# Kernel tuning notes

Hardware: AMD Instinct MI355X
Metric: run time of the kernel (lower is better)

The kernel has to match this reference:

```python
import jax, jax.numpy as jnp
import numpy as np

B, S, E, NH = 1, 2048, 1024, 8
DH = E // NH
EPS = 1e-6


def setup_inputs() -> dict:
    key = jax.random.key(0)
    ks = jax.random.split(key, 7)
    q = jax.random.normal(ks[0], (B, S, E), dtype=jnp.float32)
    k = jax.random.normal(ks[1], (B, S, E), dtype=jnp.float32)
    v = jax.random.normal(ks[2], (B, S, E), dtype=jnp.float32)
    # gate projections (original inits kernel=0; use small random to keep math non-degenerate)
    Wi = jax.random.normal(ks[3], (3 * E, NH), dtype=jnp.float32) * 0.02
    bi = jax.random.normal(ks[4], (NH,), dtype=jnp.float32) * 0.1
    Wf = jax.random.normal(ks[5], (3 * E, NH), dtype=jnp.float32) * 0.02
    bf = jnp.linspace(3.0, 6.0, NH, dtype=jnp.float32)  # bias_linspace_initializer(3,6)
    ln_scale = jnp.ones((E,), dtype=jnp.float32)
    return {"q": q, "k": k, "v": v, "Wi": Wi, "bi": bi, "Wf": Wf, "bf": bf, "ln_scale": ln_scale}


def _mlstm_forward(q, k, v, Wi, bi, Wf, bf, ln_scale):
    # gate preactivations: (B, NH, S, 1)
    gate_in = jnp.concatenate([q, k, v], axis=-1)  # (B, S, 3E)
    i_pre = jnp.transpose(gate_in @ Wi + bi, (0, 2, 1))[..., None]
    f_pre = jnp.transpose(gate_in @ Wf + bf, (0, 2, 1))[..., None]

    # heads: (B, NH, S, DH)
    qh = jnp.transpose(q.reshape(B, S, NH, DH), (0, 2, 1, 3))
    kh = jnp.transpose(k.reshape(B, S, NH, DH), (0, 2, 1, 3))
    vh = jnp.transpose(v.reshape(B, S, NH, DH), (0, 2, 1, 3))

    # cumulative log forget gates -> decay matrix fm[i,j] = sum_{t=j+1..i} log_sigmoid(f_t)
    log_fg = jax.nn.log_sigmoid(f_pre)                  # (B, NH, S, 1)
    cum = jnp.cumsum(log_fg, axis=2)[..., 0]            # (B, NH, S)
    fm = cum[:, :, :, None] - cum[:, :, None, :]        # (B, NH, S, S)

    mask = jnp.tril(jnp.ones((S, S), dtype=bool))
    log_D = jnp.where(mask, fm + i_pre[..., 0][:, :, None, :], -jnp.inf)  # + igate of column j

    max_log_D = jnp.max(log_D, axis=-1, keepdims=True)  # row-wise stabilizer (B, NH, S, 1)
    D = jnp.exp(log_D - max_log_D)

    qk = jnp.einsum("bhsd,bhtd->bhst", qh, kh) / jnp.sqrt(jnp.float32(DH))
    C = qk * D
    normalizer = jnp.maximum(jnp.abs(C.sum(axis=-1, keepdims=True)), jnp.exp(-max_log_D))
    h = jnp.einsum("bhst,bhtd->bhsd", C / (normalizer + EPS), vh)  # (B, NH, S, DH)

    # per-head layernorm over DH, scale of size E reshaped per head, no bias
    mu = h.mean(axis=-1, keepdims=True)
    var = h.var(axis=-1, keepdims=True)
    h_norm = (h - mu) * jax.lax.rsqrt(var + EPS) * ln_scale.reshape(1, NH, 1, DH)

    return jnp.transpose(h_norm, (0, 2, 1, 3)).reshape(B, S, E)


def reference(q, k, v, Wi, bi, Wf, bf, ln_scale):
    return _mlstm_forward(q, k, v, Wi, bi, Wf, bf, ln_scale)
```

## Files before the change

kernel.cpp:

```cpp
#include <hip/hip_runtime.h>
#include <math.h>

namespace {
constexpr int S  = 2048;
constexpr int E  = 1024;
constexpr int NH = 8;
constexpr int DH = 128;
constexpr float EPSF = 1e-6f;
constexpr float INV_LN2 = 1.4426950408889634f;
}

typedef short short8 __attribute__((ext_vector_type(8)));
typedef float f32x16 __attribute__((ext_vector_type(16)));
typedef float f32x4  __attribute__((ext_vector_type(4)));

__device__ __forceinline__ unsigned short f2bf(float x) {
  unsigned int u = __float_as_uint(x);
  unsigned int r = (u + 0x7fffu + ((u >> 16) & 1u)) >> 16;
  return (unsigned short)r;
}

__device__ __forceinline__ void async_copy16(const void* g, void* l) {
  __builtin_amdgcn_global_load_lds(
      (const __attribute__((address_space(1))) unsigned int*)g,
      (__attribute__((address_space(3))) unsigned int*)l, 16, 0, 0);
}

__global__ __launch_bounds__(256) void convert_kernel(
    const float* __restrict__ q, const float* __restrict__ k, const float* __restrict__ v,
    const float* __restrict__ Wi, const float* __restrict__ Wf,
    unsigned short* __restrict__ qb, unsigned short* __restrict__ kb,
    unsigned short* __restrict__ vt, unsigned short* __restrict__ wt2)
{
  const int b = blockIdx.x;
  const int tid = threadIdx.x;
  if (b < 512) {
    __shared__ float Ts[64][65];
    const int j0 = (b & 31) * 64;
    const int d0 = ((b >> 5) & 1) * 64;
    const int h  = b >> 6;
    const int c = tid & 63, r4 = tid >> 6;
    #pragma unroll
    for (int rr = 0; rr < 16; ++rr) {
      int r = r4*16 + rr;
      Ts[r][c] = v[(size_t)(j0 + r)*E + h*DH + d0 + c];
    }
    __syncthreads();
    #pragma unroll
    for (int rr = 0; rr < 16; ++rr) {
      int r = r4*16 + rr;
      vt[(size_t)(h*DH + d0 + r)*S + j0 + c] = f2bf(Ts[c][r]);
    }
  } else if (b < 1024) {
    const int bb = b - 512;
    constexpr int N4 = S*E/4;
    const float4* src = (bb < 256) ? (const float4*)q : (const float4*)k;
    ushort4* dst = (bb < 256) ? (ushort4*)qb : (ushort4*)kb;
    const int b0 = (bb & 255);
    for (int i = b0*256 + tid; i < N4; i += 256*256) {
      float4 x = src[i];
      ushort4 o;
      o.x = f2bf(x.x); o.y = f2bf(x.y); o.z = f2bf(x.z); o.w = f2bf(x.w);
      dst[i] = o;
    }
  } else {
    for (int idx = tid; idx < 16*3*E; idx += 256) {
      int n = idx / (3*E), e = idx - n*(3*E);
      float val = (n < 8) ? Wi[e*NH + n] : Wf[e*NH + (n-8)];
      wt2[idx] = f2bf(val);
    }
  }
}

__global__ __launch_bounds__(256) void gates_kernel(
    const float* __restrict__ q, const float* __restrict__ k, const float* __restrict__ v,
    const unsigned short* __restrict__ wt2, float* __restrict__ partial)
{
  const int mt = blockIdx.x, p = blockIdx.y;
  const float* src = (p == 0) ? q : (p == 1) ? k : v;
  const int wv = threadIdx.x >> 6, lane = threadIdx.x & 63;
  const int m0 = (mt*4 + wv)*16;
  const int tr = lane & 15;
  const int ks = (lane >> 4) * 8;
  f32x4 acc = {0.f, 0.f, 0.f, 0.f};
  for (int e0 = 0; e0 < E; e0 += 32) {
    const float* ap = src + (size_t)(m0 + tr)*E + e0 + ks;
    float4 a0 = *reinterpret_cast<const float4*>(ap);
    float4 a1 = *reinterpret_cast<const float4*>(ap + 4);
    short8 af;
    af[0] = (short)f2bf(a0.x); af[1] = (short)f2bf(a0.y);
    af[2] = (short)f2bf(a0.z); af[3] = (short)f2bf(a0.w);
    af[4] = (short)f2bf(a1.x); af[5] = (short)f2bf(a1.y);
    af[6] = (short)f2bf(a1.z); af[7] = (short)f2bf(a1.w);
    short8 bf8 = *reinterpret_cast<const short8*>(wt2 + (size_t)tr*(3*E) + p*E + e0 + ks);
    acc = __builtin_amdgcn_mfma_f32_16x16x32_bf16(af, bf8, acc, 0, 0, 0);
  }
  const int n = lane & 15, rbase = (lane >> 4) * 4;
  #pragma unroll
  for (int r = 0; r < 4; ++r)
    partial[(size_t)(p*16 + n)*S + m0 + rbase + r] = acc[r];
}

__global__ __launch_bounds__(256) void scan_kernel(
    const float* __restrict__ partial,
    const float* __restrict__ bi, const float* __restrict__ bfg,
    float* __restrict__ a2_out, float* __restrict__ m2_out)
{
  const int h = blockIdx.x, tid = threadIdx.x;
  const int lane = tid & 63, wv = tid >> 6;
  constexpr int PER = S / 256;
  const int bt = tid * PER;
  __shared__ float wred[4], wmax[4];

  float ipv[PER], c[PER];
  float run = 0.f;
  #pragma unroll
  for (int u = 0; u < PER; u++) {
    int t = bt + u;
    float ip = bi[h], fp = bfg[h];
    #pragma unroll
    for (int p = 0; p < 3; ++p) {
      ip += partial[(size_t)(p*16 + h)*S + t];
      fp += partial[(size_t)(p*16 + 8 + h)*S + t];
    }
    ipv[u] = ip;
    float ls = fminf(fp, 0.f) - log1pf(__expf(-fabsf(fp)));
    run += ls; c[u] = run;
  }
  float s = run;
  #pragma unroll
  for (int off = 1; off < 64; off <<= 1) {
    float t = __shfl_up(s, off);
    if (lane >= off) s += t;
  }
  if (lane == 63) wred[wv] = s;
  __syncthreads();
  float wpre = 0.f;
  for (int i = 0; i < wv; i++) wpre += wred[i];
  const float excl = wpre + (s - run);

  float av[PER], mloc[PER];
  float lm = -INFINITY;
  #pragma unroll
  for (int u = 0; u < PER; u++) {
    c[u] += excl;
    av[u] = ipv[u] - c[u];
    lm = fmaxf(lm, av[u]);
    mloc[u] = lm;
  }
  float sm_ = lm;
  #pragma unroll
  for (int off = 1; off < 64; off <<= 1) {
    float t = __shfl_up(sm_, off);
    if (lane >= off) sm_ = fmaxf(sm_, t);
  }
  if (lane == 63) wmax[wv] = sm_;
  __syncthreads();
  float wpm = -INFINITY;
  for (int i = 0; i < wv; i++) wpm = fmaxf(wpm, wmax[i]);
  float prev = __shfl_up(sm_, 1);
  if (lane == 0) prev = -INFINITY;
  const float exclm = fmaxf(wpm, prev);
  #pragma unroll
  for (int u = 0; u < PER; u++) {
    float m = fmaxf(exclm, mloc[u]);
    a2_out[h*S + bt + u] = av[u] * INV_LN2;
    m2_out[h*S + bt + u] = m * INV_LN2;
  }
}

__global__ __launch_bounds__(256, 2) void attn_kernel(
    const unsigned short* __restrict__ qb, const unsigned short* __restrict__ kb,
    const unsigned short* __restrict__ vt,
    const float* __restrict__ a2g, const float* __restrict__ m2g,
    const float* __restrict__ ln, float* __restrict__ out)
{
  const int qt = 63 - (int)(blockIdx.x >> 3);
  const int h  = blockIdx.x & 7;
  const int tid = threadIdx.x;
  const int w = tid >> 6, lane = tid & 63, l31 = lane & 31, half = lane >> 5;
  const int qi0 = qt * 32;
  const int niter = (qt + 4) >> 2;
  const int jcol_off = 32*w + l31;

  __shared__ short Klds[128*128];
  __shared__ short Vlds[128*128];
  __shared__ short Psm[32*136];
  __shared__ float mrow[32];
  float* Hs = (float*)Klds;

  if (tid < 32) mrow[tid] = m2g[h*S + qi0 + tid];

  short8 qf[8];
  #pragma unroll
  for (int s = 0; s < 8; ++s)
    qf[s] = *reinterpret_cast<const short8*>(
        qb + (size_t)(qi0 + l31)*E + h*DH + 16*s + 8*half);

  __syncthreads();
  float mreg[16];
  #pragma unroll
  for (int r = 0; r < 16; ++r) mreg[r] = mrow[(r&3) + 8*(r>>2) + 4*half];

  f32x16 acc = {0,0,0,0,0,0,0,0,0,0,0,0,0,0,0,0};

  const int lrow4 = lane >> 4;
  const int jb    = lane & 15;
  const int kq_row = 32*w + l31;
  const int kq_swz = kq_row & 15;

  for (int jt = 0; jt < niter; ++jt) {
    const int j0 = jt * 128;
    __syncthreads();

    #pragma unroll
    for (int i = 0; i < 8; ++i) {
      const int ii  = w*8 + i;
      const int row = ii*4 + lrow4;
      const int cc  = jb ^ (row & 15);
      async_copy16(kb + (size_t)(j0 + row)*E + h*DH + cc*8, &Klds[ii*512]);
      async_copy16(vt + (size_t)(h*DH + row)*S + j0 + cc*8, &Vlds[ii*512]);
    }
    const float ajv = a2g[h*S + j0 + jcol_off];
    __syncthreads();

    f32x16 qk = {0,0,0,0,0,0,0,0,0,0,0,0,0,0,0,0};
    #pragma unroll
    for (int s = 0; s < 8; ++s) {
      short8 kf = *reinterpret_cast<const short8*>(
          &Klds[kq_row*128 + ((2*s + half) ^ kq_swz) * 8]);
      qk = __builtin_amdgcn_mfma_f32_32x32x16_bf16(qf[s], kf, qk, 0, 0, 0);
    }
    const int jcol = j0 + jcol_off;
    #pragma unroll
    for (int r = 0; r < 16; ++r) {
      const int iloc = (r&3) + 8*(r>>2) + 4*half;
      float pv = (jcol <= qi0 + iloc) ? qk[r] * exp2f(ajv - mreg[r]) : 0.f;
      Psm[iloc*136 + jcol_off] = (short)f2bf(pv);
    }
    __syncthreads();

    #pragma unroll
    for (int s = 0; s < 8; ++s) {
      short8 pf = *reinterpret_cast<const short8*>(&Psm[l31*136 + 16*s + 8*half]);
      short8 vf = *reinterpret_cast<const short8*>(
          &Vlds[kq_row*128 + ((2*s + half) ^ kq_swz) * 8]);
      acc = __builtin_amdgcn_mfma_f32_32x32x16_bf16(pf, vf, acc, 0, 0, 0);
    }
  }

  __syncthreads();
  #pragma unroll
  for (int r = 0; r < 16; ++r)
    Hs[((r&3) + 8*(r>>2) + 4*half)*132 + 32*w + l31] = acc[r];
  __syncthreads();
  {
    const int row = tid >> 3, seg = tid & 7;
    float vals[16];
    #pragma unroll
    for (int c4 = 0; c4 < 4; ++c4) {
      float4 v4 = *reinterpret_cast<const float4*>(&Hs[row*132 + seg*16 + c4*4]);
      vals[c4*4+0]=v4.x; vals[c4*4+1]=v4.y; vals[c4*4+2]=v4.z; vals[c4*4+3]=v4.w;
    }
    float s1 = 0.f, s2 = 0.f;
    #pragma unroll
    for (int c = 0; c < 16; ++c) { s1 += vals[c]; s2 = fmaf(vals[c], vals[c], s2); }
    #pragma unroll
    for (int off = 1; off < 8; off <<= 1) {
      s1 += __shfl_xor(s1, off);
      s2 += __shfl_xor(s2, off);
    }
    const float mu = s1 * (1.f/128.f);
    float var = fmaxf(s2 * (1.f/128.f) - mu*mu, 0.f);
    const float rs = rsqrtf(var + EPSF);
    const size_t ob = (size_t)(qi0 + row)*E + h*DH + seg*16;
    #pragma unroll
    for (int c = 0; c < 16; ++c)
      out[ob + c] = (vals[c] - mu) * rs * ln[h*DH + seg*16 + c];
  }
}

extern "C" void kernel_launch(void* const* d_in, const int* in_sizes, int n_in,
                              void* d_out, int out_size, void* d_ws, size_t ws_size,
                              hipStream_t stream) {
  const float* q  = (const float*)d_in[0];
  const float* k  = (const float*)d_in[1];
  const float* v  = (const float*)d_in[2];
  const float* Wi = (const float*)d_in[3];
  const float* bi = (const float*)d_in[4];
  const float* Wf = (const float*)d_in[5];
  const float* bf = (const float*)d_in[6];
  const float* ln = (const float*)d_in[7];
  float* out = (float*)d_out;

  char* base = (char*)d_ws;
  unsigned short* qb  = (unsigned short*)(base);
  unsigned short* kb  = (unsigned short*)(base + (size_t)S*E*2);
  unsigned short* vt  = (unsigned short*)(base + (size_t)S*E*4);
  unsigned short* wt2 = (unsigned short*)(base + (size_t)S*E*6);
  float* partial = (float*)(base + (size_t)S*E*6 + 16*3*E*2);
  float* a2 = partial + (size_t)48*S;
  float* m2 = a2 + NH*S;

  convert_kernel<<<dim3(1025), dim3(256), 0, stream>>>(q, k, v, Wi, Wf, qb, kb, vt, wt2);
  gates_kernel<<<dim3(32, 3), dim3(256), 0, stream>>>(q, k, v, wt2, partial);
  scan_kernel<<<dim3(NH), dim3(256), 0, stream>>>(partial, bi, bf, a2, m2);
  attn_kernel<<<dim3(512), dim3(256), 0, stream>>>(qb, kb, vt, a2, m2, ln, out);
}
```

Baseline: 159.6 us.

## Split long causal attention rows across two blocks and combine partials

Query tiles in the upper half (qt>=32) are now split into two blocks that each process half of the key tiles. Each half writes an unnormalized partial output, and a new combine kernel sums the two halves and applies the layernorm. This evens out per-block work along the causal triangle. The gates kernel now loops over q, k and v itself and writes ipre and log-sigmoid values directly, which shortens the scan. The weight transpose is spread across 16 blocks. The costs are an extra launch and a round trip of the partial outputs through global memory.

```diff
diff --git a/kernel.cpp b/kernel.cpp
--- a/kernel.cpp
+++ b/kernel.cpp
@@ -64,69 +64,70 @@
       dst[i] = o;
     }
   } else {
-    for (int idx = tid; idx < 16*3*E; idx += 256) {
-      int n = idx / (3*E), e = idx - n*(3*E);
+    const int n = b - 1024;
+    for (int e = tid; e < 3*E; e += 256) {
       float val = (n < 8) ? Wi[e*NH + n] : Wf[e*NH + (n-8)];
-      wt2[idx] = f2bf(val);
+      wt2[(size_t)n*(3*E) + e] = f2bf(val);
     }
   }
 }
 
 __global__ __launch_bounds__(256) void gates_kernel(
     const float* __restrict__ q, const float* __restrict__ k, const float* __restrict__ v,
-    const unsigned short* __restrict__ wt2, float* __restrict__ partial)
-{
-  const int mt = blockIdx.x, p = blockIdx.y;
-  const float* src = (p == 0) ? q : (p == 1) ? k : v;
+    const unsigned short* __restrict__ wt2,
+    const float* __restrict__ bi, const float* __restrict__ bfg,
+    float* __restrict__ ipre, float* __restrict__ lsf)
+{
   const int wv = threadIdx.x >> 6, lane = threadIdx.x & 63;
-  const int m0 = (mt*4 + wv)*16;
+  const int m0 = (blockIdx.x*4 + wv)*16;
   const int tr = lane & 15;
   const int ks = (lane >> 4) * 8;
   f32x4 acc = {0.f, 0.f, 0.f, 0.f};
-  for (int e0 = 0; e0 < E; e0 += 32) {
-    const float* ap = src + (size_t)(m0 + tr)*E + e0 + ks;
-    float4 a0 = *reinterpret_cast<const float4*>(ap);
-    float4 a1 = *reinterpret_cast<const float4*>(ap + 4);
-    short8 af;
-    af[0] = (short)f2bf(a0.x); af[1] = (short)f2bf(a0.y);
-    af[2] = (short)f2bf(a0.z); af[3] = (short)f2bf(a0.w);
-    af[4] = (short)f2bf(a1.x); af[5] = (short)f2bf(a1.y);
-    af[6] = (short)f2bf(a1.z); af[7] = (short)f2bf(a1.w);
-    short8 bf8 = *reinterpret_cast<const short8*>(wt2 + (size_t)tr*(3*E) + p*E + e0 + ks);
-    acc = __builtin_amdgcn_mfma_f32_16x16x32_bf16(af, bf8, acc, 0, 0, 0);
+  const float* srcs[3] = {q, k, v};
+  #pragma unroll
+  for (int p = 0; p < 3; ++p) {
+    const float* src = srcs[p];
+    for (int e0 = 0; e0 < E; e0 += 32) {
+      const float* ap = src + (size_t)(m0 + tr)*E + e0 + ks;
+      float4 a0 = *reinterpret_cast<const float4*>(ap);
+      float4 a1 = *reinterpret_cast<const float4*>(ap + 4);
+      short8 af;
+      af[0] = (short)f2bf(a0.x); af[1] = (short)f2bf(a0.y);
+      af[2] = (short)f2bf(a0.z); af[3] = (short)f2bf(a0.w);
+      af[4] = (short)f2bf(a1.x); af[5] = (short)f2bf(a1.y);
+      af[6] = (short)f2bf(a1.z); af[7] = (short)f2bf(a1.w);
+      short8 bf8 = *reinterpret_cast<const short8*>(wt2 + (size_t)tr*(3*E) + p*E + e0 + ks);
+      acc = __builtin_amdgcn_mfma_f32_16x16x32_bf16(af, bf8, acc, 0, 0, 0);
+    }
   }
   const int n = lane & 15, rbase = (lane >> 4) * 4;
   #pragma unroll
-  for (int r = 0; r < 4; ++r)
-    partial[(size_t)(p*16 + n)*S + m0 + rbase + r] = acc[r];
+  for (int r = 0; r < 4; ++r) {
+    int t = m0 + rbase + r;
+    float val = acc[r];
+    if (n < 8) {
+      ipre[n*S + t] = val + bi[n];
+    } else {
+      float fp = val + bfg[n-8];
+      lsf[(n-8)*S + t] = fminf(fp, 0.f) - log1pf(__expf(-fabsf(fp)));
+    }
+  }
 }
 
 __global__ __launch_bounds__(256) void scan_kernel(
-    const float* __restrict__ partial,
-    const float* __restrict__ bi, const float* __restrict__ bfg,
+    const float* __restrict__ ipre, const float* __restrict__ lsf,
     float* __restrict__ a2_out, float* __restrict__ m2_out)
 {
   const int h = blockIdx.x, tid = threadIdx.x;
   const int lane = tid & 63, wv = tid >> 6;
   constexpr int PER = S / 256;
-  const int bt = tid * PER;
+  const int base = h*S + tid*PER;
   __shared__ float wred[4], wmax[4];
 
-  float ipv[PER], c[PER];
+  float c[PER];
   float run = 0.f;
   #pragma unroll
-  for (int u = 0; u < PER; u++) {
-    int t = bt + u;
-    float ip = bi[h], fp = bfg[h];
-    #pragma unroll
-    for (int p = 0; p < 3; ++p) {
-      ip += partial[(size_t)(p*16 + h)*S + t];
-      fp += partial[(size_t)(p*16 + 8 + h)*S + t];
-    }
-    ipv[u] = ip;
-    float ls = fminf(fp, 0.f) - log1pf(__expf(-fabsf(fp)));
-    run += ls; c[u] = run;
-  }
+  for (int u = 0; u < PER; u++) { run += lsf[base+u]; c[u] = run; }
   float s = run;
   #pragma unroll
   for (int off = 1; off < 64; off <<= 1) {
@@ -144,7 +145,7 @@
   #pragma unroll
   for (int u = 0; u < PER; u++) {
     c[u] += excl;
-    av[u] = ipv[u] - c[u];
+    av[u] = ipre[base+u] - c[u];
     lm = fmaxf(lm, av[u]);
     mloc[u] = lm;
   }
@@ -164,8 +165,8 @@
   #pragma unroll
   for (int u = 0; u < PER; u++) {
     float m = fmaxf(exclm, mloc[u]);
-    a2_out[h*S + bt + u] = av[u] * INV_LN2;
-    m2_out[h*S + bt + u] = m * INV_LN2;
+    a2_out[base+u] = av[u] * INV_LN2;
+    m2_out[base+u] = m * INV_LN2;
   }
 }
 
@@ -173,14 +174,20 @@
     const unsigned short* __restrict__ qb, const unsigned short* __restrict__ kb,
     const unsigned short* __restrict__ vt,
     const float* __restrict__ a2g, const float* __restrict__ m2g,
-    const float* __restrict__ ln, float* __restrict__ out)
-{
-  const int qt = 63 - (int)(blockIdx.x >> 3);
-  const int h  = blockIdx.x & 7;
+    const float* __restrict__ ln, float* __restrict__ opart, float* __restrict__ out)
+{
+  const int b = blockIdx.x;
+  int h, qt, part;
+  if (b < 512) { h = b & 7; qt = 63 - (b >> 3); part = 0; }
+  else { int i = b - 512; h = i & 7; qt = 63 - (i >> 3); part = 1; }
+  const int nspl = (qt >= 32) ? 2 : 1;
+  const int N = (qt + 4) >> 2;
+  const int jt_lo = (part == 1) ? (N >> 1) : 0;
+  const int jt_hi = (nspl == 2 && part == 0) ? (N >> 1) : N;
+
   const int tid = threadIdx.x;
   const int w = tid >> 6, lane = tid & 63, l31 = lane & 31, half = lane >> 5;
   const int qi0 = qt * 32;
-  const int niter = (qt + 4) >> 2;
   const int jcol_off = 32*w + l31;
 
   __shared__ short Klds[128*128];
@@ -209,10 +216,9 @@
   const int kq_row = 32*w + l31;
   const int kq_swz = kq_row & 15;
 
-  for (int jt = 0; jt < niter; ++jt) {
+  for (int jt = jt_lo; jt < jt_hi; ++jt) {
     const int j0 = jt * 128;
     __syncthreads();
-
     #pragma unroll
     for (int i = 0; i < 8; ++i) {
       const int ii  = w*8 + i;
@@ -239,7 +245,6 @@
       Psm[iloc*136 + jcol_off] = (short)f2bf(pv);
     }
     __syncthreads();
-
     #pragma unroll
     for (int s = 0; s < 8; ++s) {
       short8 pf = *reinterpret_cast<const short8*>(&Psm[l31*136 + 16*s + 8*half]);
@@ -249,6 +254,16 @@
     }
   }
 
+  if (nspl == 2) {
+    float* dst = opart + ((size_t)((qt - 32)*8 + h)*2 + part)*(32*128);
+    #pragma unroll
+    for (int r = 0; r < 16; ++r) {
+      const int iloc = (r&3) + 8*(r>>2) + 4*half;
+      dst[iloc*128 + 32*w + l31] = acc[r];
+    }
+    return;
+  }
+
   __syncthreads();
   #pragma unroll
   for (int r = 0; r < 16; ++r)
@@ -278,6 +293,42 @@
     for (int c = 0; c < 16; ++c)
       out[ob + c] = (vals[c] - mu) * rs * ln[h*DH + seg*16 + c];
   }
+}
+
+__global__ __launch_bounds__(256) void combine_kernel(
+    const float* __restrict__ opart, const float* __restrict__ ln,
+    float* __restrict__ out)
+{
+  const int t = blockIdx.x;
+  const int qt = 32 + (t >> 3);
+  const int h  = t & 7;
+  const float* p0 = opart + (size_t)((qt - 32)*8 + h)*2*(32*128);
+  const float* p1 = p0 + 32*128;
+  const int tid = threadIdx.x;
+  const int row = tid >> 3, seg = tid & 7;
+  float vals[16];
+  #pragma unroll
+  for (int c4 = 0; c4 < 4; ++c4) {
+    float4 a = *reinterpret_cast<const float4*>(&p0[row*128 + seg*16 + c4*4]);
+    float4 b = *reinterpret_cast<const float4*>(&p1[row*128 + seg*16 + c4*4]);
+    vals[c4*4+0] = a.x + b.x; vals[c4*4+1] = a.y + b.y;
+    vals[c4*4+2] = a.z + b.z; vals[c4*4+3] = a.w + b.w;
+  }
+  float s1 = 0.f, s2 = 0.f;
+  #pragma unroll
+  for (int c = 0; c < 16; ++c) { s1 += vals[c]; s2 = fmaf(vals[c], vals[c], s2); }
+  #pragma unroll
+  for (int off = 1; off < 8; off <<= 1) {
+    s1 += __shfl_xor(s1, off);
+    s2 += __shfl_xor(s2, off);
+  }
+  const float mu = s1 * (1.f/128.f);
+  float var = fmaxf(s2 * (1.f/128.f) - mu*mu, 0.f);
+  const float rs = rsqrtf(var + EPSF);
+  const size_t ob = (size_t)(qt*32 + row)*E + h*DH + seg*16;
+  #pragma unroll
+  for (int c = 0; c < 16; ++c)
+    out[ob + c] = (vals[c] - mu) * rs * ln[h*DH + seg*16 + c];
 }
 
 extern "C" void kernel_launch(void* const* d_in, const int* in_sizes, int n_in,
@@ -298,12 +349,16 @@
   unsigned short* kb  = (unsigned short*)(base + (size_t)S*E*2);
   unsigned short* vt  = (unsigned short*)(base + (size_t)S*E*4);
   unsigned short* wt2 = (unsigned short*)(base + (size_t)S*E*6);
-  float* partial = (float*)(base + (size_t)S*E*6 + 16*3*E*2);
-  float* a2 = partial + (size_t)48*S;
-  float* m2 = a2 + NH*S;
-
-  convert_kernel<<<dim3(1025), dim3(256), 0, stream>>>(q, k, v, Wi, Wf, qb, kb, vt, wt2);
-  gates_kernel<<<dim3(32, 3), dim3(256), 0, stream>>>(q, k, v, wt2, partial);
-  scan_kernel<<<dim3(NH), dim3(256), 0, stream>>>(partial, bi, bf, a2, m2);
-  attn_kernel<<<dim3(512), dim3(256), 0, stream>>>(qb, kb, vt, a2, m2, ln, out);
-}
+  float* fbase = (float*)(base + (size_t)S*E*6 + 16*3*E*2);
+  float* ipre = fbase;
+  float* lsf  = fbase + 1*NH*S;
+  float* a2   = fbase + 2*NH*S;
+  float* m2   = fbase + 3*NH*S;
+  float* opart = fbase + 4*NH*S;
+
+  convert_kernel<<<dim3(1040), dim3(256), 0, stream>>>(q, k, v, Wi, Wf, qb, kb, vt, wt2);
+  gates_kernel<<<dim3(32), dim3(256), 0, stream>>>(q, k, v, wt2, bi, bf, ipre, lsf);
+  scan_kernel<<<dim3(NH), dim3(256), 0, stream>>>(ipre, lsf, a2, m2);
+  attn_kernel<<<dim3(768), dim3(256), 0, stream>>>(qb, kb, vt, a2, m2, ln, opart, out);
+  combine_kernel<<<dim3(256), dim3(256), 0, stream>>>(opart, ln, out);
+}
```

Result: no change. 157.0 us (-1.6%).

## Fuse gate GEMM into preprocessing kernel and split long attention rows across blocks

Applied to the files above, without the earlier changes.

The gate projection GEMM now runs inside the conversion kernel: each block handles 16 rows over all of E, reduces across waves in LDS, and writes input-gate preactivations and log-sigmoid forget terms directly. This removes one kernel launch and the partial buffer. The attention kernel splits the causal key loop for the longest query tiles into two halves run by separate blocks. Their partial outputs are merged through a workspace buffer and an atomic ticket, and the last block to finish applies the layernorm. This is meant to balance the triangular workload across CUs, at the cost of extra global traffic and fence/atomic synchronisation.

```diff
diff --git a/kernel.cpp b/kernel.cpp
--- a/kernel.cpp
+++ b/kernel.cpp
@@ -26,19 +26,72 @@
       (__attribute__((address_space(3))) unsigned int*)l, 16, 0, 0);
 }
 
-__global__ __launch_bounds__(256) void convert_kernel(
+__global__ __launch_bounds__(256) void merged_pre_kernel(
     const float* __restrict__ q, const float* __restrict__ k, const float* __restrict__ v,
     const float* __restrict__ Wi, const float* __restrict__ Wf,
+    const float* __restrict__ bi, const float* __restrict__ bfg,
     unsigned short* __restrict__ qb, unsigned short* __restrict__ kb,
-    unsigned short* __restrict__ vt, unsigned short* __restrict__ wt2)
+    unsigned short* __restrict__ vt,
+    float* __restrict__ ipre, float* __restrict__ lsf, int* __restrict__ cnt)
 {
+  __shared__ __align__(16) char smem[38912];
   const int b = blockIdx.x;
   const int tid = threadIdx.x;
-  if (b < 512) {
-    __shared__ float Ts[64][65];
-    const int j0 = (b & 31) * 64;
-    const int d0 = ((b >> 5) & 1) * 64;
-    const int h  = b >> 6;
+
+  if (b < 128) {
+    const int wv = tid >> 6, lane = tid & 63;
+    const int m0 = b * 16;
+    const int tr = lane & 15;
+    const int ks = (lane >> 4) * 8;
+    unsigned short* Wl = (unsigned short*)smem + wv * (16*264);
+    float* red = (float*)(smem + 33792);
+    f32x4 acc = {0.f, 0.f, 0.f, 0.f};
+    const float* srcs[3] = {q, k, v};
+    for (int p = 0; p < 3; ++p) {
+      for (int i = lane; i < 2048; i += 64) {
+        int el = i >> 3, n = i & 7;
+        int eg = p*E + wv*256 + el;
+        Wl[n*264 + el]     = f2bf(Wi[eg*NH + n]);
+        Wl[(n+8)*264 + el] = f2bf(Wf[eg*NH + n]);
+      }
+      const float* src = srcs[p];
+      for (int s = 0; s < 8; ++s) {
+        const float* ap = src + (size_t)(m0 + tr)*E + wv*256 + s*32 + ks;
+        float4 a0 = *reinterpret_cast<const float4*>(ap);
+        float4 a1 = *reinterpret_cast<const float4*>(ap + 4);
+        short8 af;
+        af[0] = (short)f2bf(a0.x); af[1] = (short)f2bf(a0.y);
+        af[2] = (short)f2bf(a0.z); af[3] = (short)f2bf(a0.w);
+        af[4] = (short)f2bf(a1.x); af[5] = (short)f2bf(a1.y);
+        af[6] = (short)f2bf(a1.z); af[7] = (short)f2bf(a1.w);
+        short8 bf8 = *reinterpret_cast<const short8*>(&Wl[tr*264 + s*32 + ks]);
+        acc = __builtin_amdgcn_mfma_f32_16x16x32_bf16(af, bf8, acc, 0, 0, 0);
+      }
+    }
+    #pragma unroll
+    for (int r = 0; r < 4; ++r)
+      red[wv*256 + (lane&15)*16 + (lane>>4)*4 + r] = acc[r];
+    __syncthreads();
+    {
+      const int n = tid & 15, m = tid >> 4;
+      float val = red[0*256 + n*16 + m] + red[1*256 + n*16 + m]
+                + red[2*256 + n*16 + m] + red[3*256 + n*16 + m];
+      const int t = m0 + m;
+      if (n < 8) {
+        ipre[n*S + t] = val + bi[n];
+      } else {
+        float fp = val + bfg[n-8];
+        lsf[(n-8)*S + t] = fminf(fp, 0.f) - log1pf(__expf(-fabsf(fp)));
+      }
+    }
+  } else if (b == 128) {
+    if (tid < 256) cnt[tid] = 0;
+  } else if (b < 641) {
+    float (*Ts)[65] = (float(*)[65])smem;
+    const int bb = b - 129;
+    const int j0 = (bb & 31) * 64;
+    const int d0 = ((bb >> 5) & 1) * 64;
+    const int h  = bb >> 6;
     const int c = tid & 63, r4 = tid >> 6;
     #pragma unroll
     for (int rr = 0; rr < 16; ++rr) {
@@ -51,8 +104,8 @@
       int r = r4*16 + rr;
       vt[(size_t)(h*DH + d0 + r)*S + j0 + c] = f2bf(Ts[c][r]);
     }
-  } else if (b < 1024) {
-    const int bb = b - 512;
+  } else {
+    const int bb = b - 641;
     constexpr int N4 = S*E/4;
     const float4* src = (bb < 256) ? (const float4*)q : (const float4*)k;
     ushort4* dst = (bb < 256) ? (ushort4*)qb : (ushort4*)kb;
@@ -63,70 +116,23 @@
       o.x = f2bf(x.x); o.y = f2bf(x.y); o.z = f2bf(x.z); o.w = f2bf(x.w);
       dst[i] = o;
     }
-  } else {
-    for (int idx = tid; idx < 16*3*E; idx += 256) {
-      int n = idx / (3*E), e = idx - n*(3*E);
-      float val = (n < 8) ? Wi[e*NH + n] : Wf[e*NH + (n-8)];
-      wt2[idx] = f2bf(val);
-    }
-  }
-}
-
-__global__ __launch_bounds__(256) void gates_kernel(
-    const float* __restrict__ q, const float* __restrict__ k, const float* __restrict__ v,
-    const unsigned short* __restrict__ wt2, float* __restrict__ partial)
-{
-  const int mt = blockIdx.x, p = blockIdx.y;
-  const float* src = (p == 0) ? q : (p == 1) ? k : v;
-  const int wv = threadIdx.x >> 6, lane = threadIdx.x & 63;
-  const int m0 = (mt*4 + wv)*16;
-  const int tr = lane & 15;
-  const int ks = (lane >> 4) * 8;
-  f32x4 acc = {0.f, 0.f, 0.f, 0.f};
-  for (int e0 = 0; e0 < E; e0 += 32) {
-    const float* ap = src + (size_t)(m0 + tr)*E + e0 + ks;
-    float4 a0 = *reinterpret_cast<const float4*>(ap);
-    float4 a1 = *reinterpret_cast<const float4*>(ap + 4);
-    short8 af;
-    af[0] = (short)f2bf(a0.x); af[1] = (short)f2bf(a0.y);
-    af[2] = (short)f2bf(a0.z); af[3] = (short)f2bf(a0.w);
-    af[4] = (short)f2bf(a1.x); af[5] = (short)f2bf(a1.y);
-    af[6] = (short)f2bf(a1.z); af[7] = (short)f2bf(a1.w);
-    short8 bf8 = *reinterpret_cast<const short8*>(wt2 + (size_t)tr*(3*E) + p*E + e0 + ks);
-    acc = __builtin_amdgcn_mfma_f32_16x16x32_bf16(af, bf8, acc, 0, 0, 0);
-  }
-  const int n = lane & 15, rbase = (lane >> 4) * 4;
-  #pragma unroll
-  for (int r = 0; r < 4; ++r)
-    partial[(size_t)(p*16 + n)*S + m0 + rbase + r] = acc[r];
+  }
 }
 
 __global__ __launch_bounds__(256) void scan_kernel(
-    const float* __restrict__ partial,
-    const float* __restrict__ bi, const float* __restrict__ bfg,
+    const float* __restrict__ ipre, const float* __restrict__ lsf,
     float* __restrict__ a2_out, float* __restrict__ m2_out)
 {
   const int h = blockIdx.x, tid = threadIdx.x;
   const int lane = tid & 63, wv = tid >> 6;
   constexpr int PER = S / 256;
-  const int bt = tid * PER;
+  const int base = h*S + tid*PER;
   __shared__ float wred[4], wmax[4];
 
-  float ipv[PER], c[PER];
+  float c[PER];
   float run = 0.f;
   #pragma unroll
-  for (int u = 0; u < PER; u++) {
-    int t = bt + u;
-    float ip = bi[h], fp = bfg[h];
-    #pragma unroll
-    for (int p = 0; p < 3; ++p) {
-      ip += partial[(size_t)(p*16 + h)*S + t];
-      fp += partial[(size_t)(p*16 + 8 + h)*S + t];
-    }
-    ipv[u] = ip;
-    float ls = fminf(fp, 0.f) - log1pf(__expf(-fabsf(fp)));
-    run += ls; c[u] = run;
-  }
+  for (int u = 0; u < PER; u++) { run += lsf[base+u]; c[u] = run; }
   float s = run;
   #pragma unroll
   for (int off = 1; off < 64; off <<= 1) {
@@ -144,7 +150,7 @@
   #pragma unroll
   for (int u = 0; u < PER; u++) {
     c[u] += excl;
-    av[u] = ipv[u] - c[u];
+    av[u] = ipre[base+u] - c[u];
     lm = fmaxf(lm, av[u]);
     mloc[u] = lm;
   }
@@ -164,8 +170,8 @@
   #pragma unroll
   for (int u = 0; u < PER; u++) {
     float m = fmaxf(exclm, mloc[u]);
-    a2_out[h*S + bt + u] = av[u] * INV_LN2;
-    m2_out[h*S + bt + u] = m * INV_LN2;
+    a2_out[base+u] = av[u] * INV_LN2;
+    m2_out[base+u] = m * INV_LN2;
   }
 }
 
@@ -173,20 +179,31 @@
     const unsigned short* __restrict__ qb, const unsigned short* __restrict__ kb,
     const unsigned short* __restrict__ vt,
     const float* __restrict__ a2g, const float* __restrict__ m2g,
-    const float* __restrict__ ln, float* __restrict__ out)
+    const float* __restrict__ ln, float* __restrict__ opart,
+    int* __restrict__ cnt, float* __restrict__ out)
 {
-  const int qt = 63 - (int)(blockIdx.x >> 3);
-  const int h  = blockIdx.x & 7;
+  const int h   = blockIdx.x & 7;
+  const int idx = blockIdx.x >> 3;
+  int qt, part, nspl;
+  if (idx < 56)      { qt = 63 - (idx >> 1);        part = idx & 1; nspl = 2; }
+  else if (idx < 64) { qt = 31 - (idx - 56);        part = 0;       nspl = 1; }
+  else if (idx < 72) { qt = 35 - ((idx - 64) >> 1); part = idx & 1; nspl = 2; }
+  else               { qt = 23 - (idx - 72);        part = 0;       nspl = 1; }
+  const int N = (qt + 4) >> 2;
+  const int jt_lo = part ? (N >> 1) : 0;
+  const int jt_hi = (nspl == 2 && part == 0) ? (N >> 1) : N;
+  const int pairid = (qt - 32)*8 + h;
+
   const int tid = threadIdx.x;
   const int w = tid >> 6, lane = tid & 63, l31 = lane & 31, half = lane >> 5;
   const int qi0 = qt * 32;
-  const int niter = (qt + 4) >> 2;
   const int jcol_off = 32*w + l31;
 
   __shared__ short Klds[128*128];
   __shared__ short Vlds[128*128];
   __shared__ short Psm[32*136];
   __shared__ float mrow[32];
+  __shared__ int ticket_s;
   float* Hs = (float*)Klds;
 
   if (tid < 32) mrow[tid] = m2g[h*S + qi0 + tid];
@@ -209,10 +226,9 @@
   const int kq_row = 32*w + l31;
   const int kq_swz = kq_row & 15;
 
-  for (int jt = 0; jt < niter; ++jt) {
+  for (int jt = jt_lo; jt < jt_hi; ++jt) {
     const int j0 = jt * 128;
     __syncthreads();
-
     #pragma unroll
     for (int i = 0; i < 8; ++i) {
       const int ii  = w*8 + i;
@@ -239,7 +255,6 @@
       Psm[iloc*136 + jcol_off] = (short)f2bf(pv);
     }
     __syncthreads();
-
     #pragma unroll
     for (int s = 0; s < 8; ++s) {
       short8 pf = *reinterpret_cast<const short8*>(&Psm[l31*136 + 16*s + 8*half]);
@@ -254,30 +269,51 @@
   for (int r = 0; r < 16; ++r)
     Hs[((r&3) + 8*(r>>2) + 4*half)*132 + 32*w + l31] = acc[r];
   __syncthreads();
-  {
-    const int row = tid >> 3, seg = tid & 7;
-    float vals[16];
+
+  const int row = tid >> 3, seg = tid & 7;
+  float vals[16];
+  #pragma unroll
+  for (int c4 = 0; c4 < 4; ++c4) {
+    float4 v4 = *reinterpret_cast<const float4*>(&Hs[row*132 + seg*16 + c4*4]);
+    vals[c4*4+0]=v4.x; vals[c4*4+1]=v4.y; vals[c4*4+2]=v4.z; vals[c4*4+3]=v4.w;
+  }
+
+  if (nspl == 2) {
+    float* dst = opart + ((size_t)pairid*2 + part)*(32*128);
+    #pragma unroll
+    for (int c4 = 0; c4 < 4; ++c4)
+      *reinterpret_cast<float4*>(&dst[row*128 + seg*16 + c4*4]) =
+          *reinterpret_cast<const float4*>(&Hs[row*132 + seg*16 + c4*4]);
+    __threadfence();
+    __syncthreads();
+    if (tid == 0) ticket_s = atomicAdd(&cnt[pairid], 1);
+    __syncthreads();
+    if (ticket_s == 0) return;
+    __threadfence();
+    const float* oth = opart + ((size_t)pairid*2 + (1 - part))*(32*128);
     #pragma unroll
     for (int c4 = 0; c4 < 4; ++c4) {
-      float4 v4 = *reinterpret_cast<const float4*>(&Hs[row*132 + seg*16 + c4*4]);
-      vals[c4*4+0]=v4.x; vals[c4*4+1]=v4.y; vals[c4*4+2]=v4.z; vals[c4*4+3]=v4.w;
-    }
-    float s1 = 0.f, s2 = 0.f;
-    #pragma unroll
-    for (int c = 0; c < 16; ++c) { s1 += vals[c]; s2 = fmaf(vals[c], vals[c], s2); }
-    #pragma unroll
-    for (int off = 1; off < 8; off <<= 1) {
-      s1 += __shfl_xor(s1, off);
-      s2 += __shfl_xor(s2, off);
-    }
-    const float mu = s1 * (1.f/128.f);
-    float var = fmaxf(s2 * (1.f/128.f) - mu*mu, 0.f);
-    const float rs = rsqrtf(var + EPSF);
-    const size_t ob = (size_t)(qi0 + row)*E + h*DH + seg*16;
-    #pragma unroll
-    for (int c = 0; c < 16; ++c)
-      out[ob + c] = (vals[c] - mu) * rs * ln[h*DH + seg*16 + c];
-  }
+      float4 o = *reinterpret_cast<const float4*>(&oth[row*128 + seg*16 + c4*4]);
+      vals[c4*4+0] += o.x; vals[c4*4+1] += o.y;
+      vals[c4*4+2] += o.z; vals[c4*4+3] += o.w;
+    }
+  }
+
+  float s1 = 0.f, s2 = 0.f;
+  #pragma unroll
+  for (int c = 0; c < 16; ++c) { s1 += vals[c]; s2 = fmaf(vals[c], vals[c], s2); }
+  #pragma unroll
+  for (int off = 1; off < 8; off <<= 1) {
+    s1 += __shfl_xor(s1, off);
+    s2 += __shfl_xor(s2, off);
+  }
+  const float mu = s1 * (1.f/128.f);
+  float var = fmaxf(s2 * (1.f/128.f) - mu*mu, 0.f);
+  const float rs = rsqrtf(var + EPSF);
+  const size_t ob = (size_t)(qi0 + row)*E + h*DH + seg*16;
+  #pragma unroll
+  for (int c = 0; c < 16; ++c)
+    out[ob + c] = (vals[c] - mu) * rs * ln[h*DH + seg*16 + c];
 }
 
 extern "C" void kernel_launch(void* const* d_in, const int* in_sizes, int n_in,
@@ -297,13 +333,16 @@
   unsigned short* qb  = (unsigned short*)(base);
   unsigned short* kb  = (unsigned short*)(base + (size_t)S*E*2);
   unsigned short* vt  = (unsigned short*)(base + (size_t)S*E*4);
-  unsigned short* wt2 = (unsigned short*)(base + (size_t)S*E*6);
-  float* partial = (float*)(base + (size_t)S*E*6 + 16*3*E*2);
-  float* a2 = partial + (size_t)48*S;
-  float* m2 = a2 + NH*S;
-
-  convert_kernel<<<dim3(1025), dim3(256), 0, stream>>>(q, k, v, Wi, Wf, qb, kb, vt, wt2);
-  gates_kernel<<<dim3(32, 3), dim3(256), 0, stream>>>(q, k, v, wt2, partial);
-  scan_kernel<<<dim3(NH), dim3(256), 0, stream>>>(partial, bi, bf, a2, m2);
-  attn_kernel<<<dim3(512), dim3(256), 0, stream>>>(qb, kb, vt, a2, m2, ln, out);
-}
+  float* fbase = (float*)(base + (size_t)S*E*6);
+  float* ipre  = fbase;
+  float* lsf   = fbase + 1*NH*S;
+  float* a2    = fbase + 2*NH*S;
+  float* m2    = fbase + 3*NH*S;
+  float* opart = fbase + 4*NH*S;
+  int*   cnt   = (int*)(opart + (size_t)256*2*32*128);
+
+  merged_pre_kernel<<<dim3(1153), dim3(256), 0, stream>>>(
+      q, k, v, Wi, Wf, bi, bf, qb, kb, vt, ipre, lsf, cnt);
+  scan_kernel<<<dim3(NH), dim3(256), 0, stream>>>(ipre, lsf, a2, m2);
+  attn_kernel<<<dim3(768), dim3(256), 0, stream>>>(qb, kb, vt, a2, m2, ln, opart, cnt, out);
+}
```

Measured after the change: 260.1 us. +63.0%, slower.
